# Kernel tuning notes

Measured on AMD Instinct MI355X. Metric: run time of the kernel, lower is better.

The kernel has to match this reference:

```python
import jax, jax.numpy as jnp
import numpy as np

HEAD_SIZE = 64
N_EMBD = 128
B, T = 16, 2048


def setup_inputs() -> dict:
    key = jax.random.key(0)
    ks = jax.random.split(key, 7)
    s = 1.0 / np.sqrt(N_EMBD)
    return {
        "x": jax.random.normal(ks[0], (B, T, N_EMBD), dtype=jnp.float32),
        "Wk": jax.random.normal(ks[1], (N_EMBD, HEAD_SIZE), dtype=jnp.float32) * s,
        "bk": jax.random.normal(ks[2], (HEAD_SIZE,), dtype=jnp.float32) * s,
        "Wq": jax.random.normal(ks[3], (N_EMBD, HEAD_SIZE), dtype=jnp.float32) * s,
        "bq": jax.random.normal(ks[4], (HEAD_SIZE,), dtype=jnp.float32) * s,
        "Wv": jax.random.normal(ks[5], (N_EMBD, HEAD_SIZE), dtype=jnp.float32) * s,
        "bv": jax.random.normal(ks[6], (HEAD_SIZE,), dtype=jnp.float32) * s,
    }


def reference(x, Wk, bk, Wq, bq, Wv, bv):
    # x: [B, T, C]; single-head causal attention (dropout in eval mode = identity)
    Tdim = x.shape[1]
    k = x @ Wk + bk  # [B, T, H]
    q = x @ Wq + bq  # [B, T, H]
    v = x @ Wv + bv  # [B, T, H]
    scale = jnp.asarray(k.shape[-1], x.dtype) ** -0.5
    wei = jnp.einsum("bth,bsh->bts", q, k) * scale  # [B, T, T]
    causal = jnp.tril(jnp.ones((Tdim, Tdim), dtype=bool))
    wei = jnp.where(causal, wei, -jnp.inf)
    wei = jax.nn.softmax(wei, axis=-1)
    out = jnp.einsum("bts,bsh->bth", wei, v)  # [B, T, H]
    return out
```

## Files before the change

### kernel.cpp

```cpp
#include <hip/hip_runtime.h>
#include <hip/hip_bf16.h>
#include <math.h>

#define HS 64
#define NE 128
#define TSEQ 2048

typedef short s8v __attribute__((ext_vector_type(8)));
typedef float f4v __attribute__((ext_vector_type(4)));

__device__ __forceinline__ unsigned short f2bf(float f) {
    unsigned int u = __float_as_uint(f);
    u += 0x7FFFu + ((u >> 16) & 1u);
    return (unsigned short)(u >> 16);
}

__device__ __forceinline__ unsigned int pkbf(float a, float b) {
    union { __hip_bfloat162 h; unsigned int u; } cv;
    cv.h = __float22bfloat162_rn(make_float2(a, b));
    return cv.u;
}

__device__ __forceinline__ s8v mk_s8v(unsigned int a, unsigned int b,
                                      unsigned int c, unsigned int d) {
    union { unsigned int u[4]; s8v v; } cv;
    cv.u[0] = a; cv.u[1] = b; cv.u[2] = c; cv.u[3] = d;
    return cv.v;
}

__device__ __forceinline__ float fexp2(float x) {
    float r;
    asm("v_exp_f32 %0, %1" : "=v"(r) : "v"(x));
    return r;
}

__device__ __forceinline__ void glds16(const unsigned short* g, unsigned short* l) {
    __builtin_amdgcn_global_load_lds(
        (const __attribute__((address_space(1))) unsigned int*)g,
        (__attribute__((address_space(3))) unsigned int*)l,
        16, 0, 0);
}

__global__ __launch_bounds__(256) void wconv(
    const float* __restrict__ Wq, const float* __restrict__ Wk,
    const float* __restrict__ Wv, unsigned short* __restrict__ wt)
{
    const int o0 = (blockIdx.x * 256 + threadIdx.x) * 2;
    const int mat = o0 >> 13;
    const int n = (o0 >> 7) & 63;
    const int k = o0 & 127;
    const float* W = (mat == 0) ? Wq : (mat == 1) ? Wk : Wv;
    const float s = (mat == 0) ? 0.18033688f : 1.0f;
    unsigned int lo = f2bf(W[k * HS + n] * s);
    unsigned int hi = f2bf(W[(k + 1) * HS + n] * s);
    *(unsigned int*)(wt + o0) = lo | (hi << 16);
}

__global__ __launch_bounds__(256) void qkv(
    const float* __restrict__ x, const unsigned short* __restrict__ wt,
    const float* __restrict__ bq, const float* __restrict__ bk,
    const float* __restrict__ bv,
    unsigned short* __restrict__ qo, unsigned short* __restrict__ ko,
    unsigned short* __restrict__ vt)
{
    __shared__ __align__(16) unsigned short Ws[192 * 136];

    const int tid = threadIdx.x;
    const int w = tid >> 6;
    const int lane = tid & 63;
    const int quad = lane >> 4;
    const int li = lane & 15;
    const size_t blk0 = (size_t)blockIdx.x * 64;
    const size_t row0w = blk0 + (size_t)w * 16;

#pragma unroll
    for (int p = 0; p < 12; ++p) {
        const int idx = p * 256 + tid;
        const int n = idx >> 4;
        const int c = idx & 15;
        s8v d = *(const s8v*)(wt + idx * 8);
        *(s8v*)&Ws[n * 136 + c * 8] = d;
    }

    s8v a[4];
    const float* xr = x + (row0w + li) * NE + quad * 8;
#pragma unroll
    for (int ks = 0; ks < 4; ++ks) {
        float4 f0 = *(const float4*)(xr + ks * 32);
        float4 f1 = *(const float4*)(xr + ks * 32 + 4);
        a[ks] = mk_s8v(pkbf(f0.x, f0.y), pkbf(f0.z, f0.w),
                       pkbf(f1.x, f1.y), pkbf(f1.z, f1.w));
    }

    __syncthreads();

    f4v acc[12];
#pragma unroll
    for (int nt = 0; nt < 12; ++nt) acc[nt] = (f4v){0.f, 0.f, 0.f, 0.f};

#pragma unroll
    for (int nt = 0; nt < 12; ++nt) {
        const unsigned short* wr = &Ws[(nt * 16 + li) * 136 + quad * 8];
#pragma unroll
        for (int ks = 0; ks < 4; ++ks) {
            s8v bfr = *(const s8v*)(wr + ks * 32);
            acc[nt] = __builtin_amdgcn_mfma_f32_16x16x32_bf16(a[ks], bfr, acc[nt], 0, 0, 0);
        }
    }

    const size_t bidx = row0w >> 11;
    const size_t trow0 = row0w & 2047;
#pragma unroll
    for (int nt = 0; nt < 4; ++nt) {
        const float bias = bv[nt * 16 + li];
        unsigned int lo = pkbf(acc[nt + 8][0] + bias, acc[nt + 8][1] + bias);
        unsigned int hi = pkbf(acc[nt + 8][2] + bias, acc[nt + 8][3] + bias);
        *(uint2*)(vt + (bidx * HS + nt * 16 + li) * TSEQ + trow0 + quad * 4) =
            make_uint2(lo, hi);
    }

    __syncthreads();

    float* Qt = (float*)Ws;
    float* Kt = Qt + 64 * 68;
    const float sq = 0.18033688f;
    const int lrow0 = w * 16 + quad * 4;
#pragma unroll
    for (int nt = 0; nt < 4; ++nt) {
        const int col = nt * 16 + li;
        const float bq_ = bq[col] * sq;
        const float bk_ = bk[col];
#pragma unroll
        for (int r = 0; r < 4; ++r) {
            Qt[(lrow0 + r) * 68 + col] = acc[nt][r] + bq_;
            Kt[(lrow0 + r) * 68 + col] = acc[nt + 4][r] + bk_;
        }
    }

    __syncthreads();

    const int row = tid >> 2;
    const int seg = tid & 3;
    {
        const float* src = &Qt[row * 68 + seg * 16];
        float4 f0 = *(const float4*)src;
        float4 f1 = *(const float4*)(src + 4);
        float4 f2 = *(const float4*)(src + 8);
        float4 f3 = *(const float4*)(src + 12);
        s8v d0 = mk_s8v(pkbf(f0.x, f0.y), pkbf(f0.z, f0.w), pkbf(f1.x, f1.y), pkbf(f1.z, f1.w));
        s8v d1 = mk_s8v(pkbf(f2.x, f2.y), pkbf(f2.z, f2.w), pkbf(f3.x, f3.y), pkbf(f3.z, f3.w));
        unsigned short* dst = qo + (blk0 + row) * HS + seg * 16;
        *(s8v*)dst = d0;
        *(s8v*)(dst + 8) = d1;
    }
    {
        const float* src = &Kt[row * 68 + seg * 16];
        float4 f0 = *(const float4*)src;
        float4 f1 = *(const float4*)(src + 4);
        float4 f2 = *(const float4*)(src + 8);
        float4 f3 = *(const float4*)(src + 12);
        s8v d0 = mk_s8v(pkbf(f0.x, f0.y), pkbf(f0.z, f0.w), pkbf(f1.x, f1.y), pkbf(f1.z, f1.w));
        s8v d1 = mk_s8v(pkbf(f2.x, f2.y), pkbf(f2.z, f2.w), pkbf(f3.x, f3.y), pkbf(f3.z, f3.w));
        unsigned short* dst = ko + (blk0 + row) * HS + seg * 16;
        *(s8v*)dst = d0;
        *(s8v*)(dst + 8) = d1;
    }
}

__global__ __launch_bounds__(256) void attn_main(
    const unsigned short* __restrict__ qb,
    const unsigned short* __restrict__ kb,
    const unsigned short* __restrict__ vtb,
    float* __restrict__ out, float* __restrict__ pbuf, float* __restrict__ lsbuf)
{
    __shared__ unsigned short Ks[2][64 * 64];
    __shared__ unsigned short Vs[2][64 * 64];
    __shared__ __align__(16) unsigned short Ps[4][1024];

    const int tid = threadIdx.x;
    const int w = tid >> 6;
    const int lane = tid & 63;
    const int quad = lane >> 4;
    const int li = lane & 15;

    const int id = blockIdx.x;
    const int b = id / 80;
    const int u = 79 - (id - b * 80);
    int qt, c, nc;
    if (u < 8)       { qt = u;                 c = 0;            nc = 1; }
    else if (u < 24) { qt = 8 + ((u - 8) >> 1);  c = (u - 8) & 1;  nc = 2; }
    else if (u < 48) { qt = 16 + (u - 24) / 3;   c = (u - 24) % 3; nc = 3; }
    else             { qt = 24 + ((u - 48) >> 2); c = (u - 48) & 3; nc = 4; }
    const int tb = c * 8;
    const int te_ = tb + 8;
    const int te = (te_ < qt + 1) ? te_ : (qt + 1);

    const size_t base = (size_t)b * TSEQ;
    const int t0 = qt << 6;
    const int qrow = t0 + w * 16 + li;

    const unsigned short* qrp = qb + (base + qrow) * HS + quad * 8;
    s8v qf0 = *(const s8v*)qrp;
    s8v qf1 = *(const s8v*)(qrp + 32);

    const int rA = w * 8 + (lane >> 3);
    const int csw = (lane & 7) ^ (rA & 7);
    const unsigned short* kgA = kb + (base + rA) * HS + csw * 8;
    const unsigned short* kgB = kgA + 32 * HS;
    const unsigned short* vgA = vtb + ((size_t)b * HS + rA) * TSEQ + csw * 8;
    const unsigned short* vgB = vgA + 32 * TSEQ;
    const int ldsA = w * 512 + lane * 8;
    const int ldsB = 2048 + w * 512 + lane * 8;

    glds16(kgA + (size_t)tb * 4096, &Ks[0][ldsA]);
    glds16(kgB + (size_t)tb * 4096, &Ks[0][ldsB]);
    glds16(vgA + (size_t)tb * 64,   &Vs[0][ldsA]);
    glds16(vgB + (size_t)tb * 64,   &Vs[0][ldsB]);

    f4v c_o[4];
#pragma unroll
    for (int f = 0; f < 4; ++f) c_o[f] = (f4v){0.f, 0.f, 0.f, 0.f};
    float lsum = 0.f;

    char* pbse = (char*)&Ps[w][0];
    const int swz0 = (quad ^ (li & 7)) * 8;
    const int swz1 = ((4 + quad) ^ (li & 7)) * 8;

    __syncthreads();

    for (int tl = tb; tl < te; ++tl) {
        const int bi = (tl - tb) & 1;
        if (tl + 1 < te) {
            const int nb = bi ^ 1;
            glds16(kgA + (size_t)(tl + 1) * 4096, &Ks[nb][ldsA]);
            glds16(kgB + (size_t)(tl + 1) * 4096, &Ks[nb][ldsB]);
            glds16(vgA + (size_t)(tl + 1) * 64,   &Vs[nb][ldsA]);
            glds16(vgB + (size_t)(tl + 1) * 64,   &Vs[nb][ldsB]);
        }
        const unsigned short* Kc = &Ks[bi][0];
        const unsigned short* Vc = &Vs[bi][0];
        const bool diag = (tl == qt);

        float pr[4][4];
        float rs = 0.f;
#pragma unroll
        for (int kt = 0; kt < 4; ++kt) {
            const unsigned short* krow = Kc + (kt * 16 + li) * 64;
            s8v k0 = *(const s8v*)(krow + swz0);
            s8v k1 = *(const s8v*)(krow + swz1);
            f4v cst = (f4v){0.f, 0.f, 0.f, 0.f};
            cst = __builtin_amdgcn_mfma_f32_16x16x32_bf16(k0, qf0, cst, 0, 0, 0);
            cst = __builtin_amdgcn_mfma_f32_16x16x32_bf16(k1, qf1, cst, 0, 0, 0);
            if (diag) {
                const int key0 = (tl << 6) + kt * 16 + quad * 4;
#pragma unroll
                for (int rr = 0; rr < 4; ++rr)
                    if (key0 + rr > qrow) cst[rr] = -INFINITY;
            }
#pragma unroll
            for (int rr = 0; rr < 4; ++rr) {
                pr[kt][rr] = fexp2(cst[rr]);
                rs += pr[kt][rr];
            }
        }
        lsum += rs;

#pragma unroll
        for (int kt = 0; kt < 4; ++kt) {
            *(uint2*)(pbse + (kt * 2 + (quad >> 1)) * 256 + li * 16 + (quad & 1) * 8) =
                make_uint2(pkbf(pr[kt][0], pr[kt][1]), pkbf(pr[kt][2], pr[kt][3]));
        }
        s8v pf0 = *(const s8v*)(pbse + lane * 16);
        s8v pf1 = *(const s8v*)(pbse + 1024 + lane * 16);

#pragma unroll
        for (int f = 0; f < 4; ++f) {
            const unsigned short* vrow = Vc + (f * 16 + li) * 64;
            s8v v0 = *(const s8v*)(vrow + swz0);
            s8v v1 = *(const s8v*)(vrow + swz1);
            c_o[f] = __builtin_amdgcn_mfma_f32_16x16x32_bf16(v0, pf0, c_o[f], 0, 0, 0);
            c_o[f] = __builtin_amdgcn_mfma_f32_16x16x32_bf16(v1, pf1, c_o[f], 0, 0, 0);
        }

        __syncthreads();
    }

    lsum += __shfl_xor(lsum, 16);
    lsum += __shfl_xor(lsum, 32);

    if (nc == 1) {
        const float inv = 1.0f / lsum;
        float* orow = out + (base + qrow) * HS + quad * 4;
#pragma unroll
        for (int f = 0; f < 4; ++f) {
            f4v res = c_o[f];
            res[0] *= inv; res[1] *= inv; res[2] *= inv; res[3] *= inv;
            *(f4v*)(orow + f * 16) = res;
        }
    } else {
        const int local = (qt < 16) ? (qt - 8) * 2 + c
                        : (qt < 24) ? 16 + (qt - 16) * 3 + c
                                    : 40 + (qt - 24) * 4 + c;
        const int pidx = b * 72 + local;
        float* pc = pbuf + (size_t)pidx * 4096 + (w * 16 + li) * 64;
#pragma unroll
        for (int f = 0; f < 4; ++f)
            *(f4v*)(pc + f * 16 + quad * 4) = c_o[f];
        if (quad == 0)
            lsbuf[(size_t)pidx * 64 + w * 16 + li] = lsum;
    }
}

__global__ __launch_bounds__(256) void attn_reduce(
    const float* __restrict__ pbuf, const float* __restrict__ lsbuf,
    float* __restrict__ out)
{
    const int g = blockIdx.x;
    const int b = g / 24;
    const int r = g - b * 24;
    int qt, lbase, nc;
    if (r < 8)       { qt = 8 + r;        lbase = 2 * r;            nc = 2; }
    else if (r < 16) { qt = 16 + (r - 8); lbase = 16 + 3 * (r - 8); nc = 3; }
    else             { qt = 24 + (r - 16); lbase = 40 + 4 * (r - 16); nc = 4; }
    const int pidx0 = b * 72 + lbase;

    const int tid = threadIdx.x;
    const int row = tid >> 2;
    const int seg = tid & 3;

    float4 acc[4];
#pragma unroll
    for (int j = 0; j < 4; ++j) acc[j] = make_float4(0.f, 0.f, 0.f, 0.f);
    float ls = 0.f;

    for (int cc = 0; cc < nc; ++cc) {
        const float* pc = pbuf + (size_t)(pidx0 + cc) * 4096 + row * 64 + seg * 16;
#pragma unroll
        for (int j = 0; j < 4; ++j) {
            float4 v = *(const float4*)(pc + j * 4);
            acc[j].x += v.x; acc[j].y += v.y; acc[j].z += v.z; acc[j].w += v.w;
        }
        ls += lsbuf[(size_t)(pidx0 + cc) * 64 + row];
    }
    const float inv = 1.0f / ls;
    float* orow = out + ((size_t)b * TSEQ + (qt << 6) + row) * HS + seg * 16;
#pragma unroll
    for (int j = 0; j < 4; ++j) {
        *(float4*)(orow + j * 4) = make_float4(acc[j].x * inv, acc[j].y * inv,
                                               acc[j].z * inv, acc[j].w * inv);
    }
}

extern "C" void kernel_launch(void* const* d_in, const int* in_sizes, int n_in,
                              void* d_out, int out_size, void* d_ws, size_t ws_size,
                              hipStream_t stream) {
    const float* x  = (const float*)d_in[0];
    const float* Wk = (const float*)d_in[1];
    const float* bk = (const float*)d_in[2];
    const float* Wq = (const float*)d_in[3];
    const float* bq = (const float*)d_in[4];
    const float* Wv = (const float*)d_in[5];
    const float* bv = (const float*)d_in[6];
    float* outp = (float*)d_out;

    const size_t elems = (size_t)16 * TSEQ * HS;
    unsigned short* qbuf = (unsigned short*)d_ws;
    unsigned short* kbuf = qbuf + elems;
    unsigned short* vbuf = kbuf + elems;
    unsigned short* wtb  = vbuf + elems;
    float* pbuf  = (float*)(wtb + 32768);
    float* lsbuf = pbuf + (size_t)1152 * 4096;

    wconv<<<48, 256, 0, stream>>>(Wq, Wk, Wv, wtb);
    qkv<<<512, 256, 0, stream>>>(x, wtb, bq, bk, bv, qbuf, kbuf, vbuf);
    attn_main<<<1280, 256, 0, stream>>>(qbuf, kbuf, vbuf, outp, pbuf, lsbuf);
    attn_reduce<<<384, 256, 0, stream>>>(pbuf, lsbuf, outp);
}
```

Before: 116.2 us.

## Process two query tiles per block to reuse K/V loads, map batches to XCDs

```diff
diff --git a/kernel.cpp b/kernel.cpp
--- a/kernel.cpp
+++ b/kernel.cpp
@@ -167,8 +167,59 @@
     }
 }
 
+__device__ __forceinline__ void attn_tile_group(
+    const unsigned short* Kc, const unsigned short* Vc,
+    char* pbse, int lane, int quad, int li, int swz0, int swz1,
+    int tl, int dg, int qrow, s8v qf0, s8v qf1, f4v* c_o, float& lsum)
+{
+    float pr[4][4];
+    float rs = 0.f;
+#pragma unroll
+    for (int kt = 0; kt < 4; ++kt) {
+        const unsigned short* krow = Kc + (kt * 16 + li) * 64;
+        s8v k0 = *(const s8v*)(krow + swz0);
+        s8v k1 = *(const s8v*)(krow + swz1);
+        f4v cst = (f4v){0.f, 0.f, 0.f, 0.f};
+        __builtin_amdgcn_s_setprio(1);
+        cst = __builtin_amdgcn_mfma_f32_16x16x32_bf16(k0, qf0, cst, 0, 0, 0);
+        cst = __builtin_amdgcn_mfma_f32_16x16x32_bf16(k1, qf1, cst, 0, 0, 0);
+        __builtin_amdgcn_s_setprio(0);
+        if (tl == dg) {
+            const int key0 = (tl << 6) + kt * 16 + quad * 4;
+#pragma unroll
+            for (int rr = 0; rr < 4; ++rr)
+                if (key0 + rr > qrow) cst[rr] = -INFINITY;
+        }
+#pragma unroll
+        for (int rr = 0; rr < 4; ++rr) {
+            pr[kt][rr] = fexp2(cst[rr]);
+            rs += pr[kt][rr];
+        }
+    }
+    lsum += rs;
+
+#pragma unroll
+    for (int kt = 0; kt < 4; ++kt) {
+        *(uint2*)(pbse + (kt * 2 + (quad >> 1)) * 256 + li * 16 + (quad & 1) * 8) =
+            make_uint2(pkbf(pr[kt][0], pr[kt][1]), pkbf(pr[kt][2], pr[kt][3]));
+    }
+    s8v pf0 = *(const s8v*)(pbse + lane * 16);
+    s8v pf1 = *(const s8v*)(pbse + 1024 + lane * 16);
+
+#pragma unroll
+    for (int f = 0; f < 4; ++f) {
+        const unsigned short* vrow = Vc + (f * 16 + li) * 64;
+        s8v v0 = *(const s8v*)(vrow + swz0);
+        s8v v1 = *(const s8v*)(vrow + swz1);
+        __builtin_amdgcn_s_setprio(1);
+        c_o[f] = __builtin_amdgcn_mfma_f32_16x16x32_bf16(v0, pf0, c_o[f], 0, 0, 0);
+        c_o[f] = __builtin_amdgcn_mfma_f32_16x16x32_bf16(v1, pf1, c_o[f], 0, 0, 0);
+        __builtin_amdgcn_s_setprio(0);
+    }
+}
+
 __global__ __launch_bounds__(256) void attn_main(
-    const unsigned short* __restrict__ qb,
+    const unsigned short* __restrict__ qbf,
     const unsigned short* __restrict__ kb,
     const unsigned short* __restrict__ vtb,
     float* __restrict__ out, float* __restrict__ pbuf, float* __restrict__ lsbuf)
@@ -184,24 +235,33 @@
     const int li = lane & 15;
 
     const int id = blockIdx.x;
-    const int b = id / 80;
-    const int u = 79 - (id - b * 80);
-    int qt, c, nc;
-    if (u < 8)       { qt = u;                 c = 0;            nc = 1; }
-    else if (u < 24) { qt = 8 + ((u - 8) >> 1);  c = (u - 8) & 1;  nc = 2; }
-    else if (u < 48) { qt = 16 + (u - 24) / 3;   c = (u - 24) % 3; nc = 3; }
-    else             { qt = 24 + ((u - 48) >> 2); c = (u - 48) & 3; nc = 4; }
+    const int xcd = id & 7;
+    const int j = id >> 3;
+    const int b = xcd * 2 + (j >= 40);
+    const int jj = (j >= 40) ? j - 40 : j;
+    const int u = 39 - jj;
+    int qb, c, nc;
+    if (u < 4)       { qb = u;                    c = 0;             nc = 1; }
+    else if (u < 12) { qb = 4 + ((u - 4) >> 1);   c = (u - 4) & 1;   nc = 2; }
+    else if (u < 24) { qb = 8 + (u - 12) / 3;     c = (u - 12) % 3;  nc = 3; }
+    else             { qb = 12 + ((u - 24) >> 2); c = (u - 24) & 3;  nc = 4; }
     const int tb = c * 8;
-    const int te_ = tb + 8;
-    const int te = (te_ < qt + 1) ? te_ : (qt + 1);
+    const int ntile = 2 * qb + 2;
+    const int te = (tb + 8 < ntile) ? tb + 8 : ntile;
 
     const size_t base = (size_t)b * TSEQ;
-    const int t0 = qt << 6;
-    const int qrow = t0 + w * 16 + li;
-
-    const unsigned short* qrp = qb + (base + qrow) * HS + quad * 8;
-    s8v qf0 = *(const s8v*)qrp;
-    s8v qf1 = *(const s8v*)(qrp + 32);
+    const int t0 = qb << 7;
+    const int qrow0 = t0 + w * 16 + li;
+    const int qrow1 = qrow0 + 64;
+    const int d0 = 2 * qb;
+    const int d1 = 2 * qb + 1;
+
+    const unsigned short* qrp0 = qbf + (base + qrow0) * HS + quad * 8;
+    s8v qA0 = *(const s8v*)qrp0;
+    s8v qA1 = *(const s8v*)(qrp0 + 32);
+    const unsigned short* qrp1 = qrp0 + 64 * HS;
+    s8v qB0 = *(const s8v*)qrp1;
+    s8v qB1 = *(const s8v*)(qrp1 + 32);
 
     const int rA = w * 8 + (lane >> 3);
     const int csw = (lane & 7) ^ (rA & 7);
@@ -217,10 +277,13 @@
     glds16(vgA + (size_t)tb * 64,   &Vs[0][ldsA]);
     glds16(vgB + (size_t)tb * 64,   &Vs[0][ldsB]);
 
-    f4v c_o[4];
-#pragma unroll
-    for (int f = 0; f < 4; ++f) c_o[f] = (f4v){0.f, 0.f, 0.f, 0.f};
-    float lsum = 0.f;
+    f4v c_oA[4], c_oB[4];
+#pragma unroll
+    for (int f = 0; f < 4; ++f) {
+        c_oA[f] = (f4v){0.f, 0.f, 0.f, 0.f};
+        c_oB[f] = (f4v){0.f, 0.f, 0.f, 0.f};
+    }
+    float lsA = 0.f, lsB = 0.f;
 
     char* pbse = (char*)&Ps[w][0];
     const int swz0 = (quad ^ (li & 7)) * 8;
@@ -239,75 +302,55 @@
         }
         const unsigned short* Kc = &Ks[bi][0];
         const unsigned short* Vc = &Vs[bi][0];
-        const bool diag = (tl == qt);
-
-        float pr[4][4];
-        float rs = 0.f;
-#pragma unroll
-        for (int kt = 0; kt < 4; ++kt) {
-            const unsigned short* krow = Kc + (kt * 16 + li) * 64;
-            s8v k0 = *(const s8v*)(krow + swz0);
-            s8v k1 = *(const s8v*)(krow + swz1);
-            f4v cst = (f4v){0.f, 0.f, 0.f, 0.f};
-            cst = __builtin_amdgcn_mfma_f32_16x16x32_bf16(k0, qf0, cst, 0, 0, 0);
-            cst = __builtin_amdgcn_mfma_f32_16x16x32_bf16(k1, qf1, cst, 0, 0, 0);
-            if (diag) {
-                const int key0 = (tl << 6) + kt * 16 + quad * 4;
-#pragma unroll
-                for (int rr = 0; rr < 4; ++rr)
-                    if (key0 + rr > qrow) cst[rr] = -INFINITY;
-            }
-#pragma unroll
-            for (int rr = 0; rr < 4; ++rr) {
-                pr[kt][rr] = fexp2(cst[rr]);
-                rs += pr[kt][rr];
-            }
-        }
-        lsum += rs;
-
-#pragma unroll
-        for (int kt = 0; kt < 4; ++kt) {
-            *(uint2*)(pbse + (kt * 2 + (quad >> 1)) * 256 + li * 16 + (quad & 1) * 8) =
-                make_uint2(pkbf(pr[kt][0], pr[kt][1]), pkbf(pr[kt][2], pr[kt][3]));
-        }
-        s8v pf0 = *(const s8v*)(pbse + lane * 16);
-        s8v pf1 = *(const s8v*)(pbse + 1024 + lane * 16);
-
+
+        if (tl <= d0)
+            attn_tile_group(Kc, Vc, pbse, lane, quad, li, swz0, swz1,
+                            tl, d0, qrow0, qA0, qA1, c_oA, lsA);
+        attn_tile_group(Kc, Vc, pbse, lane, quad, li, swz0, swz1,
+                        tl, d1, qrow1, qB0, qB1, c_oB, lsB);
+
+        __syncthreads();
+    }
+
+    lsA += __shfl_xor(lsA, 16);
+    lsA += __shfl_xor(lsA, 32);
+    lsB += __shfl_xor(lsB, 16);
+    lsB += __shfl_xor(lsB, 32);
+
+    if (nc == 1) {
+        const float invA = 1.0f / lsA;
+        float* orowA = out + (base + qrow0) * HS + quad * 4;
 #pragma unroll
         for (int f = 0; f < 4; ++f) {
-            const unsigned short* vrow = Vc + (f * 16 + li) * 64;
-            s8v v0 = *(const s8v*)(vrow + swz0);
-            s8v v1 = *(const s8v*)(vrow + swz1);
-            c_o[f] = __builtin_amdgcn_mfma_f32_16x16x32_bf16(v0, pf0, c_o[f], 0, 0, 0);
-            c_o[f] = __builtin_amdgcn_mfma_f32_16x16x32_bf16(v1, pf1, c_o[f], 0, 0, 0);
-        }
-
-        __syncthreads();
-    }
-
-    lsum += __shfl_xor(lsum, 16);
-    lsum += __shfl_xor(lsum, 32);
-
-    if (nc == 1) {
-        const float inv = 1.0f / lsum;
-        float* orow = out + (base + qrow) * HS + quad * 4;
+            f4v res = c_oA[f];
+            res[0] *= invA; res[1] *= invA; res[2] *= invA; res[3] *= invA;
+            *(f4v*)(orowA + f * 16) = res;
+        }
+        const float invB = 1.0f / lsB;
+        float* orowB = out + (base + qrow1) * HS + quad * 4;
 #pragma unroll
         for (int f = 0; f < 4; ++f) {
-            f4v res = c_o[f];
-            res[0] *= inv; res[1] *= inv; res[2] *= inv; res[3] *= inv;
-            *(f4v*)(orow + f * 16) = res;
+            f4v res = c_oB[f];
+            res[0] *= invB; res[1] *= invB; res[2] *= invB; res[3] *= invB;
+            *(f4v*)(orowB + f * 16) = res;
         }
     } else {
-        const int local = (qt < 16) ? (qt - 8) * 2 + c
-                        : (qt < 24) ? 16 + (qt - 16) * 3 + c
-                                    : 40 + (qt - 24) * 4 + c;
-        const int pidx = b * 72 + local;
-        float* pc = pbuf + (size_t)pidx * 4096 + (w * 16 + li) * 64;
+        const int local = (qb < 8)  ? (qb - 4) * 2 + c
+                        : (qb < 12) ? 8 + (qb - 8) * 3 + c
+                                    : 20 + (qb - 12) * 4 + c;
+        const int pidx = b * 36 + local;
+        float* pc = pbuf + (size_t)pidx * 8192 + (w * 16 + li) * 64;
 #pragma unroll
         for (int f = 0; f < 4; ++f)
-            *(f4v*)(pc + f * 16 + quad * 4) = c_o[f];
-        if (quad == 0)
-            lsbuf[(size_t)pidx * 64 + w * 16 + li] = lsum;
+            *(f4v*)(pc + f * 16 + quad * 4) = c_oA[f];
+        float* pc1 = pc + 64 * 64;
+#pragma unroll
+        for (int f = 0; f < 4; ++f)
+            *(f4v*)(pc1 + f * 16 + quad * 4) = c_oB[f];
+        if (quad == 0) {
+            lsbuf[(size_t)pidx * 128 + w * 16 + li] = lsA;
+            lsbuf[(size_t)pidx * 128 + 64 + w * 16 + li] = lsB;
+        }
     }
 }
 
@@ -316,36 +359,36 @@
     float* __restrict__ out)
 {
     const int g = blockIdx.x;
-    const int b = g / 24;
-    const int r = g - b * 24;
-    int qt, lbase, nc;
-    if (r < 8)       { qt = 8 + r;        lbase = 2 * r;            nc = 2; }
-    else if (r < 16) { qt = 16 + (r - 8); lbase = 16 + 3 * (r - 8); nc = 3; }
-    else             { qt = 24 + (r - 16); lbase = 40 + 4 * (r - 16); nc = 4; }
-    const int pidx0 = b * 72 + lbase;
+    const int b = g / 12;
+    const int r = g - b * 12;
+    int qb, lbase, nc;
+    if (r < 4)      { qb = 4 + r;        lbase = 2 * r;            nc = 2; }
+    else if (r < 8) { qb = 8 + (r - 4);  lbase = 8 + 3 * (r - 4);  nc = 3; }
+    else            { qb = 12 + (r - 8); lbase = 20 + 4 * (r - 8); nc = 4; }
+    const int pidx0 = b * 36 + lbase;
 
     const int tid = threadIdx.x;
-    const int row = tid >> 2;
-    const int seg = tid & 3;
-
-    float4 acc[4];
-#pragma unroll
-    for (int j = 0; j < 4; ++j) acc[j] = make_float4(0.f, 0.f, 0.f, 0.f);
+    const int row = tid >> 1;
+    const int seg = tid & 1;
+
+    float4 acc[8];
+#pragma unroll
+    for (int j = 0; j < 8; ++j) acc[j] = make_float4(0.f, 0.f, 0.f, 0.f);
     float ls = 0.f;
 
     for (int cc = 0; cc < nc; ++cc) {
-        const float* pc = pbuf + (size_t)(pidx0 + cc) * 4096 + row * 64 + seg * 16;
-#pragma unroll
-        for (int j = 0; j < 4; ++j) {
+        const float* pc = pbuf + (size_t)(pidx0 + cc) * 8192 + row * 64 + seg * 32;
+#pragma unroll
+        for (int j = 0; j < 8; ++j) {
             float4 v = *(const float4*)(pc + j * 4);
             acc[j].x += v.x; acc[j].y += v.y; acc[j].z += v.z; acc[j].w += v.w;
         }
-        ls += lsbuf[(size_t)(pidx0 + cc) * 64 + row];
+        ls += lsbuf[(size_t)(pidx0 + cc) * 128 + row];
     }
     const float inv = 1.0f / ls;
-    float* orow = out + ((size_t)b * TSEQ + (qt << 6) + row) * HS + seg * 16;
-#pragma unroll
-    for (int j = 0; j < 4; ++j) {
+    float* orow = out + ((size_t)b * TSEQ + (qb << 7) + row) * HS + seg * 32;
+#pragma unroll
+    for (int j = 0; j < 8; ++j) {
         *(float4*)(orow + j * 4) = make_float4(acc[j].x * inv, acc[j].y * inv,
                                                acc[j].z * inv, acc[j].w * inv);
     }
@@ -369,10 +412,10 @@
     unsigned short* vbuf = kbuf + elems;
     unsigned short* wtb  = vbuf + elems;
     float* pbuf  = (float*)(wtb + 32768);
-    float* lsbuf = pbuf + (size_t)1152 * 4096;
+    float* lsbuf = pbuf + (size_t)576 * 8192;
 
     wconv<<<48, 256, 0, stream>>>(Wq, Wk, Wv, wtb);
     qkv<<<512, 256, 0, stream>>>(x, wtb, bq, bk, bv, qbuf, kbuf, vbuf);
-    attn_main<<<1280, 256, 0, stream>>>(qbuf, kbuf, vbuf, outp, pbuf, lsbuf);
-    attn_reduce<<<384, 256, 0, stream>>>(pbuf, lsbuf, outp);
-}
+    attn_main<<<640, 256, 0, stream>>>(qbuf, kbuf, vbuf, outp, pbuf, lsbuf);
+    attn_reduce<<<192, 256, 0, stream>>>(pbuf, lsbuf, outp);
+}
```

Measured after the change: 115.7 us. About the same (-0.5%).
